# Kernel optimization log

Hardware: AMD Instinct MI355X
Metric: run time of the kernel (lower is better)

The kernel has to match this reference:

```python
import jax, jax.numpy as jnp
import numpy as np
import math

B, S, E, H = 2, 2048, 2048, 16
HD = E // H // 2  # 64, per-head dim of each differential half
DEPTH = 12
LAMBDA_INIT = 0.8 - 0.6 * math.exp(-0.3 * DEPTH)
EPS = 1e-5


def setup_inputs() -> dict:
    key = jax.random.key(0)
    ks = jax.random.split(key, 10)
    sc = 0.02
    return {
        "x": jax.random.normal(ks[0], (B, S, E), jnp.float32),
        "Wq": jax.random.normal(ks[1], (E, E), jnp.float32) * sc,
        "Wk": jax.random.normal(ks[2], (E, E), jnp.float32) * sc,
        "Wv": jax.random.normal(ks[3], (E, E), jnp.float32) * sc,
        "Wo": jax.random.normal(ks[4], (E, E), jnp.float32) * sc,
        "lambda_q1": jax.random.normal(ks[5], (HD,), jnp.float32) * 0.1,
        "lambda_k1": jax.random.normal(ks[6], (HD,), jnp.float32) * 0.1,
        "lambda_q2": jax.random.normal(ks[7], (HD,), jnp.float32) * 0.1,
        "lambda_k2": jax.random.normal(ks[8], (HD,), jnp.float32) * 0.1,
        "gamma": jnp.ones((2 * HD,), jnp.float32),
    }


def _rope_interleaved(x, cos, sin):
    # x: [b, s, h, d]; cos/sin: [s, d//2]; pairs are (0,1),(2,3),...
    xe, xo = x[..., 0::2], x[..., 1::2]
    c = cos[None, :, None, :]
    s = sin[None, :, None, :]
    oe = xe * c - xo * s
    oo = xe * s + xo * c
    return jnp.stack([oe, oo], axis=-1).reshape(x.shape)


def reference(x, Wq, Wk, Wv, Wo, lambda_q1, lambda_k1, lambda_q2, lambda_k2, gamma):
    b, t, _ = x.shape
    # rotary tables (rotary dim == HD, interleaved)
    angle = 1.0 / 10000 ** jnp.linspace(0.0, 1.0, HD // 2, dtype=jnp.float32)
    freqs = jnp.arange(t, dtype=jnp.float32)[:, None] * angle  # [t, HD//2]
    cos, sin = jnp.cos(freqs), jnp.sin(freqs)

    q = (x @ Wq.T).reshape(b, t, 2 * H, HD)
    k = (x @ Wk.T).reshape(b, t, 2 * H, HD)
    v = (x @ Wv.T).reshape(b, t, H, 2 * HD)  # concat(v1, v2) along last dim

    q = _rope_interleaved(q, cos, sin)
    k = _rope_interleaved(k, cos, sin)

    q = q.reshape(b, t, H, 2, HD)
    k = k.reshape(b, t, H, 2, HD)
    q1, q2 = q[:, :, :, 0], q[:, :, :, 1]
    k1, k2 = k[:, :, :, 0], k[:, :, :, 1]

    scale = HD ** -0.5  # flash_attn default softmax scale
    # branch 1: softmax(q1 k1) @ [v1|v2]
    s1 = jnp.einsum("bthd,bshd->bhts", q1, k1) * scale
    p1 = jax.nn.softmax(s1, axis=-1)
    o1 = jnp.einsum("bhts,bshd->bthd", p1, v)  # [b,t,H,2*HD]
    # branch 2: softmax(q2 k2) @ [v1|v2]
    s2 = jnp.einsum("bthd,bshd->bhts", q2, k2) * scale
    p2 = jax.nn.softmax(s2, axis=-1)
    o2 = jnp.einsum("bhts,bshd->bthd", p2, v)

    lam1 = jnp.exp(jnp.sum(lambda_q1 * lambda_k1))
    lam2 = jnp.exp(jnp.sum(lambda_q2 * lambda_k2))
    lam = lam1 - lam2 + LAMBDA_INIT

    attn = o1 - lam * o2  # [b,t,H,2*HD]
    # RMSNorm over last dim (2*HD) with affine gamma
    rms = jax.lax.rsqrt(jnp.mean(attn * attn, axis=-1, keepdims=True) + EPS)
    attn = attn * rms * gamma
    attn = attn * (1.0 - LAMBDA_INIT)
    attn = attn.reshape(b, t, H * 2 * HD)
    return attn @ Wo.T
```

## Files before the change

kernel.cpp:

```cpp
#include <hip/hip_runtime.h>
#include <cstdint>
#include <cstddef>

typedef unsigned short u16;
typedef __attribute__((ext_vector_type(8))) short short8;
typedef __attribute__((ext_vector_type(4))) float f32x4;
typedef __attribute__((ext_vector_type(16))) float f32x16;

#define MFMA_B16(a,b,c) __builtin_amdgcn_mfma_f32_16x16x32_bf16((a),(b),(c),0,0,0)
#define MFMA32(a,b,c)  __builtin_amdgcn_mfma_f32_32x32x16_bf16((a),(b),(c),0,0,0)

#define S_LEN 2048
#define EMB 2048
#define QKV_N 6144
#define HD 64
#define LAMBDA_INIT_F 0.78360576653162f
#define ONE_MINUS_LI 0.21639423346838f
#define EXP2_SCALE 0.18033688011112042f

static __device__ __forceinline__ u16 f2bf(float f) {
  unsigned u = __float_as_uint(f);
  unsigned r = ((u >> 16) & 1u) + 0x7fffu;
  return (u16)((u + r) >> 16);
}
static __device__ __forceinline__ float bf2f(u16 h) {
  return __uint_as_float(((unsigned)h) << 16);
}
static __device__ __forceinline__ unsigned cvt_pk_bf16(float lo, float hi) {
  unsigned r;
  asm("v_cvt_pk_bf16_f32 %0, %1, %2" : "=v"(r) : "v"(lo), "v"(hi));
  return r;
}
static __device__ __forceinline__ void gload_lds16(const u16* g, u16* l) {
  __builtin_amdgcn_global_load_lds((const __attribute__((address_space(1))) void*)g,
                                   (__attribute__((address_space(3))) void*)l, 16, 0, 0);
}

__global__ void cvt_f32_bf16(const float* __restrict__ s, u16* __restrict__ d, int n4) {
  int i = blockIdx.x * 256 + threadIdx.x;
  if (i >= n4) return;
  f32x4 v = *(const f32x4*)&s[i * 4];
  unsigned lo = cvt_pk_bf16(v[0], v[1]);
  unsigned hi = cvt_pk_bf16(v[2], v[3]);
  *(unsigned long long*)&d[i * 4] = (unsigned long long)lo | ((unsigned long long)hi << 32);
}

template <int BF16OUT>
__global__ __launch_bounds__(256, 2) void gemm_bt(const u16* __restrict__ A,
                                                  const u16* __restrict__ B,
                                                  void* __restrict__ Cout,
                                                  int M, int N, int K) {
  __shared__ u16 As[128 * 32];
  __shared__ u16 Bs[128 * 32];
  const int tid = threadIdx.x;
  const int lane = tid & 63, wv = tid >> 6;
  const int bm = blockIdx.x * 128, bn = blockIdx.y * 128;
  const int wr = (wv >> 1) * 64, wc = (wv & 1) * 64;
  const int lr = lane & 15, hk = lane >> 4;

  const int r0 = tid >> 2;
  const int c0 = (tid & 3) * 8;
  const u16* ga = A + (size_t)(bm + r0) * K + c0;
  const u16* gb = B + (size_t)(bn + r0) * K + c0;
  const size_t rstep = (size_t)64 * K;

  f32x4 acc[4][4] = {};

  for (int k0 = 0; k0 < K; k0 += 32) {
    __syncthreads();
    gload_lds16(ga + k0,         &As[(tid) * 8]);
    gload_lds16(ga + rstep + k0, &As[(tid + 256) * 8]);
    gload_lds16(gb + k0,         &Bs[(tid) * 8]);
    gload_lds16(gb + rstep + k0, &Bs[(tid + 256) * 8]);
    __syncthreads();
    short8 af[4], bfv[4];
#pragma unroll
    for (int i = 0; i < 4; i++) af[i] = *(const short8*)&As[(wr + i * 16 + lr) * 32 + hk * 8];
#pragma unroll
    for (int j = 0; j < 4; j++) bfv[j] = *(const short8*)&Bs[(wc + j * 16 + lr) * 32 + hk * 8];
#pragma unroll
    for (int i = 0; i < 4; i++)
#pragma unroll
      for (int j = 0; j < 4; j++)
        acc[i][j] = MFMA_B16(af[i], bfv[j], acc[i][j]);
  }

  if (BF16OUT) {
    u16* C = (u16*)Cout;
#pragma unroll
    for (int i = 0; i < 4; i++)
#pragma unroll
      for (int j = 0; j < 4; j++)
#pragma unroll
        for (int r = 0; r < 4; r++) {
          int row = bm + wr + i * 16 + hk * 4 + r;
          int col = bn + wc + j * 16 + lr;
          C[(size_t)row * N + col] = f2bf(acc[i][j][r]);
        }
  } else {
    float* C = (float*)Cout;
#pragma unroll
    for (int i = 0; i < 4; i++)
#pragma unroll
      for (int j = 0; j < 4; j++)
#pragma unroll
        for (int r = 0; r < 4; r++) {
          int row = bm + wr + i * 16 + hk * 4 + r;
          int col = bn + wc + j * 16 + lr;
          C[(size_t)row * N + col] = acc[i][j][r];
        }
  }
}

__global__ void rope_kernel(u16* __restrict__ qkv) {
  int idx = blockIdx.x * 256 + threadIdx.x;
  int p = idx & 31;
  int u = (idx >> 5) & 63;
  int m = idx >> 11;
  int t = m & (S_LEN - 1);
  int col = (u < 32) ? (u * 64 + 2 * p) : (EMB + (u - 32) * 64 + 2 * p);
  u16* ptr = qkv + (size_t)m * QKV_N + col;
  unsigned v = *(unsigned*)ptr;
  float xe = bf2f((u16)(v & 0xffff));
  float xo = bf2f((u16)(v >> 16));
  float w = expf((float)p * (-9.210340371976184f / 31.0f));
  float ang = (float)t * w;
  float sn, cs;
  sincosf(ang, &sn, &cs);
  float oe = xe * cs - xo * sn;
  float oo = xe * sn + xo * cs;
  *(unsigned*)ptr = (unsigned)f2bf(oe) | (((unsigned)f2bf(oo)) << 16);
}

#define SW(row, colByte) ((((row)) << 7) + ((colByte) ^ (((row) & 7) << 4)))

#define QKT(Kc, Q0, Q1, Q2, Q3, KT, Pc, LSUM)                                    \
  do {                                                                           \
    f32x16 s = {};                                                               \
    s = MFMA32(*(const short8*)((Kc) + SW((KT) * 32 + l31, 0  + hi16)), Q0, s);  \
    s = MFMA32(*(const short8*)((Kc) + SW((KT) * 32 + l31, 32 + hi16)), Q1, s);  \
    s = MFMA32(*(const short8*)((Kc) + SW((KT) * 32 + l31, 64 + hi16)), Q2, s);  \
    s = MFMA32(*(const short8*)((Kc) + SW((KT) * 32 + l31, 96 + hi16)), Q3, s);  \
    _Pragma("unroll") for (int r = 0; r < 16; r += 4) {                          \
      float e0 = __builtin_amdgcn_exp2f(s[r]     * EXP2_SCALE);                  \
      float e1 = __builtin_amdgcn_exp2f(s[r + 1] * EXP2_SCALE);                  \
      float e2 = __builtin_amdgcn_exp2f(s[r + 2] * EXP2_SCALE);                  \
      float e3 = __builtin_amdgcn_exp2f(s[r + 3] * EXP2_SCALE);                  \
      LSUM += (e0 + e1) + (e2 + e3);                                             \
      unsigned lo_ = cvt_pk_bf16(e0, e1);                                        \
      unsigned hi_ = cvt_pk_bf16(e2, e3);                                        \
      *(unsigned long long*)((Pc) + SW(l31, (KT) * 64 + (r >> 2) * 16 + hi8)) =  \
          (unsigned long long)lo_ | ((unsigned long long)hi_ << 32);             \
    }                                                                            \
  } while (0)

#define PVD(DT, O1, O2)                                                          \
  do {                                                                           \
    short8 va0 = *(const short8*)(VTc + SW((DT) * 32 + l31, 0  + hi16));         \
    short8 va1 = *(const short8*)(VTc + SW((DT) * 32 + l31, 32 + hi16));         \
    short8 va2 = *(const short8*)(VTc + SW((DT) * 32 + l31, 64 + hi16));         \
    short8 va3 = *(const short8*)(VTc + SW((DT) * 32 + l31, 96 + hi16));         \
    O1 = MFMA32(va0, p1f0, O1); O1 = MFMA32(va1, p1f1, O1);                      \
    O1 = MFMA32(va2, p1f2, O1); O1 = MFMA32(va3, p1f3, O1);                      \
    O2 = MFMA32(va0, p2f0, O2); O2 = MFMA32(va1, p2f1, O2);                      \
    O2 = MFMA32(va2, p2f2, O2); O2 = MFMA32(va3, p2f3, O2);                      \
  } while (0)

__global__ __launch_bounds__(256, 2) void attn_kernel(
    const u16* __restrict__ qkv, u16* __restrict__ attnb,
    const float* __restrict__ lq1, const float* __restrict__ lk1,
    const float* __restrict__ lq2, const float* __restrict__ lk2,
    const float* __restrict__ gamma) {
  __shared__ u16 K1s[64 * 64];
  __shared__ u16 K2s[64 * 64];
  __shared__ u16 VTs[128 * 64];
  __shared__ u16 Ps[2 * 2 * 32 * 64];
  __shared__ float Lr[2][2][2][32];
  __shared__ float Sr[2][2][32];

  const int g = blockIdx.x;
  const int xcd = g & 7;
  const int gi = g >> 3;
  const int bh = xcd * 4 + (gi >> 5);
  const int qt = gi & 31;
  const int b = bh >> 4, h = bh & 15;

  const int tid = threadIdx.x, lane = tid & 63, wv = tid >> 6;
  const int qg = wv >> 1;
  const int dh = wv & 1;
  const int l31 = lane & 31;
  const int hi16 = (lane >> 5) * 16;
  const int hi8 = (lane >> 5) * 8;
  const int hi4 = (lane >> 5) * 4;

  float d1 = lq1[lane] * lk1[lane];
  float d2 = lq2[lane] * lk2[lane];
#pragma unroll
  for (int off = 32; off; off >>= 1) { d1 += __shfl_xor(d1, off); d2 += __shfl_xor(d2, off); }
  const float lam = __expf(d1) - __expf(d2) + LAMBDA_INIT_F;

  const int qbase = qt * 64 + qg * 32;
  const u16* qp1 = qkv + (size_t)(b * S_LEN + qbase + l31) * QKV_N + (2 * h) * 64;
  const u16* qp2 = qp1 + 64;
  short8 q1f0 = *(const short8*)(qp1 + hi8);
  short8 q1f1 = *(const short8*)(qp1 + 16 + hi8);
  short8 q1f2 = *(const short8*)(qp1 + 32 + hi8);
  short8 q1f3 = *(const short8*)(qp1 + 48 + hi8);
  short8 q2f0 = *(const short8*)(qp2 + hi8);
  short8 q2f1 = *(const short8*)(qp2 + 16 + hi8);
  short8 q2f2 = *(const short8*)(qp2 + 32 + hi8);
  short8 q2f3 = *(const short8*)(qp2 + 48 + hi8);

  f32x16 o1t0 = {}, o1t1 = {}, o2t0 = {}, o2t1 = {};
  float l1p = 0.f, l2p = 0.f;

  const int gl_row = wv * 8 + (lane >> 3);
  const int gl_cb  = ((lane & 7) ^ (lane >> 3)) * 8;
  u16* k1d = &K1s[(wv * 8) * 64 + lane * 8];
  u16* k2d = &K2s[(wv * 8) * 64 + lane * 8];

  const int vkv = (tid & 31) * 2;
  const int vd0 = (tid >> 5) * 8;

  const u16* kb1 = qkv + (size_t)b * S_LEN * QKV_N + EMB + (2 * h) * 64;
  const u16* kb2 = kb1 + 64;
  const u16* vbp = qkv + (size_t)b * S_LEN * QKV_N + 2 * EMB + h * 128;

  char* K1c = (char*)K1s;
  char* K2c = (char*)K2s;
  char* VTc = (char*)VTs;
  char* P1c = (char*)&Ps[(qg * 2 + 0) * 32 * 64];
  char* P2c = (char*)&Ps[(qg * 2 + 1) * 32 * 64];

  for (int kv0 = 0; kv0 < S_LEN; kv0 += 64) {
    __syncthreads();
    {
      const u16* g1 = kb1 + (size_t)(kv0 + gl_row) * QKV_N + gl_cb;
      const u16* g2 = kb2 + (size_t)(kv0 + gl_row) * QKV_N + gl_cb;
      gload_lds16(g1, k1d);
      gload_lds16(g1 + (size_t)32 * QKV_N, k1d + 32 * 64);
      gload_lds16(g2, k2d);
      gload_lds16(g2 + (size_t)32 * QKV_N, k2d + 32 * 64);
    }
    {
      const u16* vs = vbp + (size_t)(kv0 + vkv) * QKV_N + vd0;
      short8 a0 = *(const short8*)vs;
      short8 a1 = *(const short8*)(vs + QKV_N);
      short8 b0 = *(const short8*)(vs + 64);
      short8 b1 = *(const short8*)(vs + QKV_N + 64);
#pragma unroll
      for (int j = 0; j < 8; j++) {
        unsigned pk0 = (unsigned)(u16)a0[j] | (((unsigned)(u16)a1[j]) << 16);
        *(unsigned*)(VTc + SW(vd0 + j, vkv * 2)) = pk0;
        unsigned pk1 = (unsigned)(u16)b0[j] | (((unsigned)(u16)b1[j]) << 16);
        *(unsigned*)(VTc + SW(vd0 + 64 + j, vkv * 2)) = pk1;
      }
    }
    __syncthreads();

    QKT(K1c, q1f0, q1f1, q1f2, q1f3, dh, P1c, l1p);
    QKT(K2c, q2f0, q2f1, q2f2, q2f3, dh, P2c, l2p);
    __syncthreads();

    short8 p1f0 = *(const short8*)(P1c + SW(l31, 0  + hi16));
    short8 p1f1 = *(const short8*)(P1c + SW(l31, 32 + hi16));
    short8 p1f2 = *(const short8*)(P1c + SW(l31, 64 + hi16));
    short8 p1f3 = *(const short8*)(P1c + SW(l31, 96 + hi16));
    short8 p2f0 = *(const short8*)(P2c + SW(l31, 0  + hi16));
    short8 p2f1 = *(const short8*)(P2c + SW(l31, 32 + hi16));
    short8 p2f2 = *(const short8*)(P2c + SW(l31, 64 + hi16));
    short8 p2f3 = *(const short8*)(P2c + SW(l31, 96 + hi16));

    PVD(dh * 2 + 0, o1t0, o2t0);
    PVD(dh * 2 + 1, o1t1, o2t1);
  }

  float l1 = l1p + __shfl_xor(l1p, 32);
  float l2 = l2p + __shfl_xor(l2p, 32);
  if (lane < 32) { Lr[qg][0][dh][l31] = l1; Lr[qg][1][dh][l31] = l2; }
  __syncthreads();
  const float inv1 = 1.f / (Lr[qg][0][0][l31] + Lr[qg][0][1][l31]);
  const float inv2 = 1.f / (Lr[qg][1][0][l31] + Lr[qg][1][1][l31]);

  float ss = 0.f;
#define COMB(O1, O2)                                                   \
  _Pragma("unroll") for (int i = 0; i < 16; i++) {                     \
    float a = O1[i] * inv1 - lam * (O2[i] * inv2);                     \
    O1[i] = a;                                                         \
    ss += a * a;                                                       \
  }
  COMB(o1t0, o2t0) COMB(o1t1, o2t1)
#undef COMB
  ss += __shfl_xor(ss, 32);
  if (lane < 32) Sr[qg][dh][l31] = ss;
  __syncthreads();
  const float SS = Sr[qg][0][l31] + Sr[qg][1][l31];
  const float sc2 = rsqrtf(SS * (1.f / 128.f) + 1e-5f) * ONE_MINUS_LI;

  u16* orow = attnb + (size_t)(b * S_LEN + qbase + l31) * EMB + h * 128;
#define WRT(O1, DT)                                                             \
  _Pragma("unroll") for (int gg = 0; gg < 4; gg++) {                            \
    int d = dh * 64 + (DT) * 32 + gg * 8 + hi4;                                 \
    f32x4 gv = *(const f32x4*)&gamma[d];                                        \
    unsigned wlo = cvt_pk_bf16(O1[4 * gg] * gv[0] * sc2, O1[4 * gg + 1] * gv[1] * sc2); \
    unsigned whi = cvt_pk_bf16(O1[4 * gg + 2] * gv[2] * sc2, O1[4 * gg + 3] * gv[3] * sc2); \
    *(unsigned long long*)&orow[d] = (unsigned long long)wlo | ((unsigned long long)whi << 32); \
  }
  WRT(o1t0, 0) WRT(o1t1, 1)
#undef WRT
}

extern "C" void kernel_launch(void* const* d_in, const int* in_sizes, int n_in,
                              void* d_out, int out_size, void* d_ws, size_t ws_size,
                              hipStream_t stream) {
  (void)in_sizes; (void)n_in; (void)out_size; (void)ws_size;
  const float* x   = (const float*)d_in[0];
  const float* Wq  = (const float*)d_in[1];
  const float* Wk  = (const float*)d_in[2];
  const float* Wv  = (const float*)d_in[3];
  const float* Wo  = (const float*)d_in[4];
  const float* lq1 = (const float*)d_in[5];
  const float* lk1 = (const float*)d_in[6];
  const float* lq2 = (const float*)d_in[7];
  const float* lk2 = (const float*)d_in[8];
  const float* gam = (const float*)d_in[9];

  char* ws = (char*)d_ws;
  u16* xb    = (u16*)(ws);
  u16* Wcat  = (u16*)(ws + 16777216);
  u16* Wob   = (u16*)(ws + 41943040);
  u16* qkv   = (u16*)(ws + 50331648);
  u16* attnb = xb;

  const int NE = EMB * EMB;
  cvt_f32_bf16<<<(2 * NE / 4 + 255) / 256, 256, 0, stream>>>(x, xb, 2 * NE / 4);
  cvt_f32_bf16<<<(NE / 4 + 255) / 256, 256, 0, stream>>>(Wq, Wcat, NE / 4);
  cvt_f32_bf16<<<(NE / 4 + 255) / 256, 256, 0, stream>>>(Wk, Wcat + NE, NE / 4);
  cvt_f32_bf16<<<(NE / 4 + 255) / 256, 256, 0, stream>>>(Wv, Wcat + 2 * NE, NE / 4);
  cvt_f32_bf16<<<(NE / 4 + 255) / 256, 256, 0, stream>>>(Wo, Wob, NE / 4);

  dim3 g1(4096 / 128, QKV_N / 128);
  gemm_bt<1><<<g1, 256, 0, stream>>>(xb, Wcat, qkv, 4096, QKV_N, EMB);

  rope_kernel<<<(4096 * 64 * 32) / 256, 256, 0, stream>>>(qkv);

  attn_kernel<<<1024, 256, 0, stream>>>(qkv, attnb, lq1, lk1, lq2, lk2, gam);

  dim3 g2(4096 / 128, EMB / 128);
  gemm_bt<0><<<g2, 256, 0, stream>>>(attnb, Wob, d_out, 4096, EMB, EMB);
}
```

Before: 355.5 us.

## Fuse conversion launches, change P/V LDS swizzle, raise attention occupancy

Merges the five fp32-to-bf16 conversion launches into one kernel that picks its source by index range, removing four launch overheads. In the attention kernel, P and V^T in LDS now use an 8-byte-granular XOR swizzle and are read as paired 64-bit loads, aiming to cut bank conflicts on the transposed V writes. Launch bounds go from 2 to 3 blocks per SIMD, which caps registers and risks spills. These are several unrelated changes in one commit.

```diff
diff --git a/kernel.cpp b/kernel.cpp
--- a/kernel.cpp
+++ b/kernel.cpp
@@ -31,18 +31,34 @@
   asm("v_cvt_pk_bf16_f32 %0, %1, %2" : "=v"(r) : "v"(lo), "v"(hi));
   return r;
 }
+static __device__ __forceinline__ short8 ld64p(const char* base, int o0, int o1) {
+  union { unsigned long long q[2]; short8 s; } x;
+  x.q[0] = *(const unsigned long long*)(base + o0);
+  x.q[1] = *(const unsigned long long*)(base + o1);
+  return x.s;
+}
 static __device__ __forceinline__ void gload_lds16(const u16* g, u16* l) {
   __builtin_amdgcn_global_load_lds((const __attribute__((address_space(1))) void*)g,
                                    (__attribute__((address_space(3))) void*)l, 16, 0, 0);
 }
 
-__global__ void cvt_f32_bf16(const float* __restrict__ s, u16* __restrict__ d, int n4) {
+__global__ void cvt_all(const float* __restrict__ x,  const float* __restrict__ Wq,
+                        const float* __restrict__ Wk, const float* __restrict__ Wv,
+                        const float* __restrict__ Wo,
+                        u16* __restrict__ xb, u16* __restrict__ Wcat, u16* __restrict__ Wob) {
+  const int NE = EMB * EMB;
+  const int NE4 = NE / 4;
   int i = blockIdx.x * 256 + threadIdx.x;
-  if (i >= n4) return;
-  f32x4 v = *(const f32x4*)&s[i * 4];
+  const float* s; u16* d; int j;
+  if (i < 2 * NE4)      { s = x;  d = xb;            j = i;           }
+  else if (i < 3 * NE4) { s = Wq; d = Wcat;          j = i - 2 * NE4; }
+  else if (i < 4 * NE4) { s = Wk; d = Wcat + NE;     j = i - 3 * NE4; }
+  else if (i < 5 * NE4) { s = Wv; d = Wcat + 2 * NE; j = i - 4 * NE4; }
+  else                  { s = Wo; d = Wob;           j = i - 5 * NE4; }
+  f32x4 v = *(const f32x4*)&s[j * 4];
   unsigned lo = cvt_pk_bf16(v[0], v[1]);
   unsigned hi = cvt_pk_bf16(v[2], v[3]);
-  *(unsigned long long*)&d[i * 4] = (unsigned long long)lo | ((unsigned long long)hi << 32);
+  *(unsigned long long*)&d[j * 4] = (unsigned long long)lo | ((unsigned long long)hi << 32);
 }
 
 template <int BF16OUT>
@@ -132,41 +148,10 @@
   *(unsigned*)ptr = (unsigned)f2bf(oe) | (((unsigned)f2bf(oo)) << 16);
 }
 
-#define SW(row, colByte) ((((row)) << 7) + ((colByte) ^ (((row) & 7) << 4)))
-
-#define QKT(Kc, Q0, Q1, Q2, Q3, KT, Pc, LSUM)                                    \
-  do {                                                                           \
-    f32x16 s = {};                                                               \
-    s = MFMA32(*(const short8*)((Kc) + SW((KT) * 32 + l31, 0  + hi16)), Q0, s);  \
-    s = MFMA32(*(const short8*)((Kc) + SW((KT) * 32 + l31, 32 + hi16)), Q1, s);  \
-    s = MFMA32(*(const short8*)((Kc) + SW((KT) * 32 + l31, 64 + hi16)), Q2, s);  \
-    s = MFMA32(*(const short8*)((Kc) + SW((KT) * 32 + l31, 96 + hi16)), Q3, s);  \
-    _Pragma("unroll") for (int r = 0; r < 16; r += 4) {                          \
-      float e0 = __builtin_amdgcn_exp2f(s[r]     * EXP2_SCALE);                  \
-      float e1 = __builtin_amdgcn_exp2f(s[r + 1] * EXP2_SCALE);                  \
-      float e2 = __builtin_amdgcn_exp2f(s[r + 2] * EXP2_SCALE);                  \
-      float e3 = __builtin_amdgcn_exp2f(s[r + 3] * EXP2_SCALE);                  \
-      LSUM += (e0 + e1) + (e2 + e3);                                             \
-      unsigned lo_ = cvt_pk_bf16(e0, e1);                                        \
-      unsigned hi_ = cvt_pk_bf16(e2, e3);                                        \
-      *(unsigned long long*)((Pc) + SW(l31, (KT) * 64 + (r >> 2) * 16 + hi8)) =  \
-          (unsigned long long)lo_ | ((unsigned long long)hi_ << 32);             \
-    }                                                                            \
-  } while (0)
-
-#define PVD(DT, O1, O2)                                                          \
-  do {                                                                           \
-    short8 va0 = *(const short8*)(VTc + SW((DT) * 32 + l31, 0  + hi16));         \
-    short8 va1 = *(const short8*)(VTc + SW((DT) * 32 + l31, 32 + hi16));         \
-    short8 va2 = *(const short8*)(VTc + SW((DT) * 32 + l31, 64 + hi16));         \
-    short8 va3 = *(const short8*)(VTc + SW((DT) * 32 + l31, 96 + hi16));         \
-    O1 = MFMA32(va0, p1f0, O1); O1 = MFMA32(va1, p1f1, O1);                      \
-    O1 = MFMA32(va2, p1f2, O1); O1 = MFMA32(va3, p1f3, O1);                      \
-    O2 = MFMA32(va0, p2f0, O2); O2 = MFMA32(va1, p2f1, O2);                      \
-    O2 = MFMA32(va2, p2f2, O2); O2 = MFMA32(va3, p2f3, O2);                      \
-  } while (0)
-
-__global__ __launch_bounds__(256, 2) void attn_kernel(
+#define SW(row, colByte)  ((((row)) << 7) + ((colByte) ^ (((row) & 7) << 4)))
+#define SW8(row, colByte) ((((row)) << 7) + ((colByte) ^ (((row) & 15) << 3)))
+
+__global__ __launch_bounds__(256, 3) void attn_kernel(
     const u16* __restrict__ qkv, u16* __restrict__ attnb,
     const float* __restrict__ lq1, const float* __restrict__ lk1,
     const float* __restrict__ lq2, const float* __restrict__ lk2,
@@ -251,28 +236,62 @@
 #pragma unroll
       for (int j = 0; j < 8; j++) {
         unsigned pk0 = (unsigned)(u16)a0[j] | (((unsigned)(u16)a1[j]) << 16);
-        *(unsigned*)(VTc + SW(vd0 + j, vkv * 2)) = pk0;
+        *(unsigned*)(VTc + SW8(vd0 + j, vkv * 2)) = pk0;
         unsigned pk1 = (unsigned)(u16)b0[j] | (((unsigned)(u16)b1[j]) << 16);
-        *(unsigned*)(VTc + SW(vd0 + 64 + j, vkv * 2)) = pk1;
+        *(unsigned*)(VTc + SW8(vd0 + 64 + j, vkv * 2)) = pk1;
       }
     }
     __syncthreads();
 
-    QKT(K1c, q1f0, q1f1, q1f2, q1f3, dh, P1c, l1p);
-    QKT(K2c, q2f0, q2f1, q2f2, q2f3, dh, P2c, l2p);
-    __syncthreads();
-
-    short8 p1f0 = *(const short8*)(P1c + SW(l31, 0  + hi16));
-    short8 p1f1 = *(const short8*)(P1c + SW(l31, 32 + hi16));
-    short8 p1f2 = *(const short8*)(P1c + SW(l31, 64 + hi16));
-    short8 p1f3 = *(const short8*)(P1c + SW(l31, 96 + hi16));
-    short8 p2f0 = *(const short8*)(P2c + SW(l31, 0  + hi16));
-    short8 p2f1 = *(const short8*)(P2c + SW(l31, 32 + hi16));
-    short8 p2f2 = *(const short8*)(P2c + SW(l31, 64 + hi16));
-    short8 p2f3 = *(const short8*)(P2c + SW(l31, 96 + hi16));
-
+#define QKT(Kc, Q0, Q1, Q2, Q3, Pc, LSUM)                                        \
+    do {                                                                         \
+      f32x16 s = {};                                                             \
+      int row = dh * 32 + l31;                                                   \
+      s = MFMA32(*(const short8*)((Kc) + SW(row, 0  + hi16)), Q0, s);            \
+      s = MFMA32(*(const short8*)((Kc) + SW(row, 32 + hi16)), Q1, s);            \
+      s = MFMA32(*(const short8*)((Kc) + SW(row, 64 + hi16)), Q2, s);            \
+      s = MFMA32(*(const short8*)((Kc) + SW(row, 96 + hi16)), Q3, s);            \
+      _Pragma("unroll") for (int r = 0; r < 16; r += 4) {                        \
+        float e0 = __builtin_amdgcn_exp2f(s[r]     * EXP2_SCALE);                \
+        float e1 = __builtin_amdgcn_exp2f(s[r + 1] * EXP2_SCALE);                \
+        float e2 = __builtin_amdgcn_exp2f(s[r + 2] * EXP2_SCALE);                \
+        float e3 = __builtin_amdgcn_exp2f(s[r + 3] * EXP2_SCALE);                \
+        LSUM += (e0 + e1) + (e2 + e3);                                           \
+        unsigned lo_ = cvt_pk_bf16(e0, e1);                                      \
+        unsigned hi_ = cvt_pk_bf16(e2, e3);                                      \
+        *(unsigned long long*)((Pc) + SW8(l31, dh * 64 + (r >> 2) * 16 + hi8)) = \
+            (unsigned long long)lo_ | ((unsigned long long)hi_ << 32);           \
+      }                                                                          \
+    } while (0)
+    QKT(K1c, q1f0, q1f1, q1f2, q1f3, P1c, l1p);
+    QKT(K2c, q2f0, q2f1, q2f2, q2f3, P2c, l2p);
+#undef QKT
+    __syncthreads();
+
+    short8 p1f0 = ld64p(P1c, SW8(l31, 0  + hi16), SW8(l31, 8   + hi16));
+    short8 p1f1 = ld64p(P1c, SW8(l31, 32 + hi16), SW8(l31, 40  + hi16));
+    short8 p1f2 = ld64p(P1c, SW8(l31, 64 + hi16), SW8(l31, 72  + hi16));
+    short8 p1f3 = ld64p(P1c, SW8(l31, 96 + hi16), SW8(l31, 104 + hi16));
+    short8 p2f0 = ld64p(P2c, SW8(l31, 0  + hi16), SW8(l31, 8   + hi16));
+    short8 p2f1 = ld64p(P2c, SW8(l31, 32 + hi16), SW8(l31, 40  + hi16));
+    short8 p2f2 = ld64p(P2c, SW8(l31, 64 + hi16), SW8(l31, 72  + hi16));
+    short8 p2f3 = ld64p(P2c, SW8(l31, 96 + hi16), SW8(l31, 104 + hi16));
+
+#define PVD(DT, O1, O2)                                                          \
+    do {                                                                         \
+      int rw = (DT) * 32 + l31;                                                  \
+      short8 va0 = ld64p(VTc, SW8(rw, 0  + hi16), SW8(rw, 8   + hi16));          \
+      short8 va1 = ld64p(VTc, SW8(rw, 32 + hi16), SW8(rw, 40  + hi16));          \
+      short8 va2 = ld64p(VTc, SW8(rw, 64 + hi16), SW8(rw, 72  + hi16));          \
+      short8 va3 = ld64p(VTc, SW8(rw, 96 + hi16), SW8(rw, 104 + hi16));          \
+      O1 = MFMA32(va0, p1f0, O1); O1 = MFMA32(va1, p1f1, O1);                    \
+      O1 = MFMA32(va2, p1f2, O1); O1 = MFMA32(va3, p1f3, O1);                    \
+      O2 = MFMA32(va0, p2f0, O2); O2 = MFMA32(va1, p2f1, O2);                    \
+      O2 = MFMA32(va2, p2f2, O2); O2 = MFMA32(va3, p2f3, O2);                    \
+    } while (0)
     PVD(dh * 2 + 0, o1t0, o2t0);
     PVD(dh * 2 + 1, o1t1, o2t1);
+#undef PVD
   }
 
   float l1 = l1p + __shfl_xor(l1p, 32);
@@ -333,11 +352,7 @@
   u16* attnb = xb;
 
   const int NE = EMB * EMB;
-  cvt_f32_bf16<<<(2 * NE / 4 + 255) / 256, 256, 0, stream>>>(x, xb, 2 * NE / 4);
-  cvt_f32_bf16<<<(NE / 4 + 255) / 256, 256, 0, stream>>>(Wq, Wcat, NE / 4);
-  cvt_f32_bf16<<<(NE / 4 + 255) / 256, 256, 0, stream>>>(Wk, Wcat + NE, NE / 4);
-  cvt_f32_bf16<<<(NE / 4 + 255) / 256, 256, 0, stream>>>(Wv, Wcat + 2 * NE, NE / 4);
-  cvt_f32_bf16<<<(NE / 4 + 255) / 256, 256, 0, stream>>>(Wo, Wob, NE / 4);
+  cvt_all<<<(6 * (NE / 4)) / 256, 256, 0, stream>>>(x, Wq, Wk, Wv, Wo, xb, Wcat, Wob);
 
   dim3 g1(4096 / 128, QKV_N / 128);
   gemm_bt<1><<<g1, 256, 0, stream>>>(xb, Wcat, qkv, 4096, QKV_N, EMB);
```

New measurement: 471.5 us. +32.6%, slower.
